# Performance work log

Measured on AMD Instinct MI355X. Metric: run time of the kernel, lower is better.

## Reference

```python
import jax, jax.numpy as jnp
import numpy as np

D_MODEL, H, D_FF = 1024, 16, 4096
B, S = 2, 2048
EPS = 1e-05


def layer_norm(x, gamma, beta):
    # Matches torch: mean and UNBIASED std over last dim, scalar gamma/beta,
    # and eps added to std (not variance).
    mean = jnp.mean(x, axis=-1, keepdims=True)
    var = jnp.sum((x - mean) ** 2, axis=-1, keepdims=True) / (x.shape[-1] - 1)
    return gamma * (x - mean) / (jnp.sqrt(var) + EPS) + beta


def setup_inputs() -> dict:
    key = jax.random.key(0)
    ks = jax.random.split(key, 16)
    sd = 1.0 / np.sqrt(D_MODEL)
    sf = 1.0 / np.sqrt(D_FF)
    return {
        "x": jax.random.normal(ks[0], (B, S, D_MODEL), jnp.float32),
        "mask": jnp.ones((1, 1, S, S), jnp.int32),
        "wq": jax.random.uniform(ks[1], (D_MODEL, D_MODEL), jnp.float32, -sd, sd),
        "bq": jax.random.uniform(ks[2], (D_MODEL,), jnp.float32, -sd, sd),
        "wk": jax.random.uniform(ks[3], (D_MODEL, D_MODEL), jnp.float32, -sd, sd),
        "bk": jax.random.uniform(ks[4], (D_MODEL,), jnp.float32, -sd, sd),
        "wv": jax.random.uniform(ks[5], (D_MODEL, D_MODEL), jnp.float32, -sd, sd),
        "bv": jax.random.uniform(ks[6], (D_MODEL,), jnp.float32, -sd, sd),
        "wo": jax.random.uniform(ks[7], (D_MODEL, D_MODEL), jnp.float32, -sd, sd),
        "bo": jax.random.uniform(ks[8], (D_MODEL,), jnp.float32, -sd, sd),
        "w1": jax.random.uniform(ks[9], (D_FF, D_MODEL), jnp.float32, -sd, sd),
        "b1": jax.random.uniform(ks[10], (D_FF,), jnp.float32, -sd, sd),
        "w2": jax.random.uniform(ks[11], (D_MODEL, D_FF), jnp.float32, -sf, sf),
        "b2": jax.random.uniform(ks[12], (D_MODEL,), jnp.float32, -sf, sf),
        "gamma1": jnp.ones((1,), jnp.float32),
        "beta1": jnp.zeros((1,), jnp.float32),
        "gamma2": jnp.ones((1,), jnp.float32),
        "beta2": jnp.zeros((1,), jnp.float32),
    }


def reference(x, mask, wq, bq, wk, bk, wv, bv, wo, bo, w1, b1, w2, b2,
              gamma1, beta1, gamma2, beta2):
    d_k = D_MODEL // H

    # --- residual 1: pre-LN self-attention ---
    xn = layer_norm(x, gamma1, beta1)
    q = (xn @ wq.T + bq).reshape(B, S, H, d_k).transpose(0, 2, 1, 3)
    k = (xn @ wk.T + bk).reshape(B, S, H, d_k).transpose(0, 2, 1, 3)
    v = (xn @ wv.T + bv).reshape(B, S, H, d_k).transpose(0, 2, 1, 3)

    scores = jnp.einsum("bhqd,bhkd->bhqk", q, k) / jnp.sqrt(
        jnp.asarray(d_k, x.dtype))
    scores = jnp.where(mask == 0, jnp.asarray(-1e9, x.dtype), scores)
    attn = jax.nn.softmax(scores, axis=-1)
    ctx = jnp.einsum("bhqk,bhkd->bhqd", attn, v)
    ctx = ctx.transpose(0, 2, 1, 3).reshape(B, S, D_MODEL)
    x = x + (ctx @ wo.T + bo)

    # --- residual 2: pre-LN feed-forward ---
    xn = layer_norm(x, gamma2, beta2)
    h = jax.nn.relu(xn @ w1.T + b1)
    x = x + (h @ w2.T + b2)
    return x
```

## Files before the change

### kernel.cpp

```cpp
#include <hip/hip_runtime.h>


typedef __bf16 bf16_t;
typedef __attribute__((ext_vector_type(8))) __bf16 bf16x8;
typedef __attribute__((ext_vector_type(4))) __bf16 bf16x4;
typedef __attribute__((ext_vector_type(2))) __bf16 bf16x2;
typedef __attribute__((ext_vector_type(4))) float f32x4;
typedef __attribute__((ext_vector_type(16))) float f32x16;
typedef __attribute__((ext_vector_type(2))) unsigned uint32x2;
typedef __attribute__((ext_vector_type(4))) unsigned uint32x4;

#define MB (1024ull * 1024ull)
#define QSCALE 0.18033688011112043f

__device__ __forceinline__ void gload_lds16(const bf16_t* g, bf16_t* l) {
    __builtin_amdgcn_global_load_lds(
        (const __attribute__((address_space(1))) void*)g,
        (__attribute__((address_space(3))) void*)l, 16, 0, 0);
}

__device__ __forceinline__ int bswz(int row) { return ((row >> 1) & 3) << 3; }

__device__ __forceinline__ int swz(int row, int col) {
    return row * 64 + ((((col >> 3) ^ row) & 7) << 3) + (col & 7);
}

__device__ __forceinline__ unsigned cvtpk(float a, float b) {
    bf16x2 v = {(__bf16)a, (__bf16)b};
    return __builtin_bit_cast(unsigned, v);
}

__global__ __launch_bounds__(256) void cvt_all(
    const float* __restrict__ wq, const float* __restrict__ wk,
    const float* __restrict__ wv, const float* __restrict__ wo,
    const float* __restrict__ w1, const float* __restrict__ w2,
    bf16_t* __restrict__ wqkv, bf16_t* __restrict__ wob, bf16_t* __restrict__ w1b,
    bf16_t* __restrict__ w2b) {
    const int b = blockIdx.x, t = threadIdx.x;
    const float* in;
    bf16_t* out;
    int i;
    if (b < 1024) { in = wq; out = wqkv; i = b * 256 + t; }
    else if (b < 2048) { in = wk; out = wqkv + 1048576; i = (b - 1024) * 256 + t; }
    else if (b < 3072) { in = wv; out = wqkv + 2097152; i = (b - 2048) * 256 + t; }
    else if (b < 4096) { in = wo; out = wob; i = (b - 3072) * 256 + t; }
    else if (b < 8192) { in = w1; out = w1b; i = (b - 4096) * 256 + t; }
    else { in = w2; out = w2b; i = (b - 8192) * 256 + t; }
    float4 v = ((const float4*)in)[i];
    bf16x4 o = {(__bf16)v.x, (__bf16)v.y, (__bf16)v.z, (__bf16)v.w};
    ((bf16x4*)out)[i] = o;
}

__global__ __launch_bounds__(256) void ln_kernel(const float* __restrict__ x,
                                                 bf16_t* __restrict__ out,
                                                 const float* __restrict__ gamma,
                                                 const float* __restrict__ beta) {
    const int lane = threadIdx.x & 63;
    const int row = blockIdx.x * 4 + (threadIdx.x >> 6);
    const float* xr = x + (size_t)row * 1024;
    float4 v[4];
    float s = 0.f;
#pragma unroll
    for (int i = 0; i < 4; ++i) {
        v[i] = ((const float4*)xr)[i * 64 + lane];
        s += v[i].x + v[i].y + v[i].z + v[i].w;
    }
#pragma unroll
    for (int o = 32; o; o >>= 1) s += __shfl_xor(s, o);
    float mean = s * (1.f / 1024.f);
    float vs = 0.f;
#pragma unroll
    for (int i = 0; i < 4; ++i) {
        float a = v[i].x - mean, b = v[i].y - mean, c = v[i].z - mean, d = v[i].w - mean;
        vs += a * a + b * b + c * c + d * d;
    }
#pragma unroll
    for (int o = 32; o; o >>= 1) vs += __shfl_xor(vs, o);
    float inv = 1.f / (sqrtf(vs * (1.f / 1023.f)) + 1e-5f);
    float g = gamma[0] * inv, bb = beta[0];
    bf16_t* orow = out + (size_t)row * 1024;
#pragma unroll
    for (int i = 0; i < 4; ++i) {
        bf16x4 ov = {(__bf16)((v[i].x - mean) * g + bb), (__bf16)((v[i].y - mean) * g + bb),
                     (__bf16)((v[i].z - mean) * g + bb), (__bf16)((v[i].w - mean) * g + bb)};
        *(bf16x4*)(orow + (i * 64 + lane) * 4) = ov;
    }
}

template <int KERN>
__global__ __launch_bounds__(512, 2) void gemm256(
    const bf16_t* __restrict__ A, const bf16_t* __restrict__ Bw, int K,
    const float* __restrict__ bias0, const float* __restrict__ bias1,
    const float* __restrict__ bias2, void* __restrict__ o0, void* __restrict__ o1,
    void* __restrict__ o2) {
    __shared__ bf16_t L[4 * 16384];
    const int t = threadIdx.x, lane = t & 63, w = t >> 6;
    const int wm = w >> 2, wn = w & 3;
    const int l15 = lane & 15, l4 = lane >> 4;
    const int bm = blockIdx.x, bn = blockIdx.y;
    const int NT = K >> 5;
    const bf16_t* Ab = A + (size_t)bm * 256 * K;
    const bf16_t* Bb = Bw + (size_t)bn * 256 * K;
    const int srow = t >> 2, pcol = (t & 3) * 8;
    f32x4 acc[8][4] = {};

    auto stageA = [&](int tt) {
        bf16_t* s = L + (tt & 3) * 16384;
        const int kb = tt * 32;
#pragma unroll
        for (int i = 0; i < 2; ++i) {
            int row = i * 128 + srow;
            int lcol = pcol ^ bswz(row);
            gload_lds16(Ab + (size_t)row * K + kb + lcol, s + i * 4096 + t * 8);
        }
    };
    auto stageB = [&](int tt) {
        bf16_t* s = L + (tt & 3) * 16384 + 8192;
        const int kb = tt * 32;
#pragma unroll
        for (int i = 0; i < 2; ++i) {
            int row = i * 128 + srow;
            int lcol = pcol ^ bswz(row);
            gload_lds16(Bb + (size_t)row * K + kb + lcol, s + i * 4096 + t * 8);
        }
    };

    stageA(0); stageB(0); stageA(1); stageB(1); stageA(2); stageB(2);
    asm volatile("s_waitcnt vmcnt(8)" ::: "memory");
    __builtin_amdgcn_s_barrier();

    for (int tt = 0; tt < NT; ++tt) {
        bf16_t* s = L + (tt & 3) * 16384;
        bf16_t* sB = s + 8192;
        bf16x8 af[4], bfr[4];
#pragma unroll
        for (int m = 0; m < 4; ++m) {
            int row = wm * 128 + m * 16 + l15;
            af[m] = *(const bf16x8*)(s + row * 32 + ((l4 * 8) ^ bswz(row)));
        }
#pragma unroll
        for (int n = 0; n < 4; ++n) {
            int row = wn * 64 + n * 16 + l15;
            bfr[n] = *(const bf16x8*)(sB + row * 32 + ((l4 * 8) ^ bswz(row)));
        }
        if (tt + 3 < NT) stageA(tt + 3);
        __builtin_amdgcn_s_barrier();
        __builtin_amdgcn_s_setprio(1);
#pragma unroll
        for (int m = 0; m < 4; ++m)
#pragma unroll
            for (int n = 0; n < 4; ++n)
                acc[m][n] = __builtin_amdgcn_mfma_f32_16x16x32_bf16(af[m], bfr[n], acc[m][n],
                                                                   0, 0, 0);
        __builtin_amdgcn_s_setprio(0);
        __builtin_amdgcn_s_barrier();
#pragma unroll
        for (int m = 0; m < 4; ++m) {
            int row = wm * 128 + 64 + m * 16 + l15;
            af[m] = *(const bf16x8*)(s + row * 32 + ((l4 * 8) ^ bswz(row)));
        }
        if (tt + 3 < NT) stageB(tt + 3);
        __builtin_amdgcn_s_barrier();
        __builtin_amdgcn_s_setprio(1);
#pragma unroll
        for (int m = 0; m < 4; ++m)
#pragma unroll
            for (int n = 0; n < 4; ++n)
                acc[4 + m][n] = __builtin_amdgcn_mfma_f32_16x16x32_bf16(af[m], bfr[n],
                                                                       acc[4 + m][n], 0, 0, 0);
        __builtin_amdgcn_s_setprio(0);
        if (tt + 3 < NT)
            asm volatile("s_waitcnt vmcnt(8)" ::: "memory");
        else if (tt + 2 < NT)
            asm volatile("s_waitcnt vmcnt(4)" ::: "memory");
        else
            asm volatile("s_waitcnt vmcnt(0)" ::: "memory");
        __builtin_amdgcn_s_barrier();
    }

    if (KERN == 1) {
        const int colb = bn * 256 + wn * 64;
        float bb[4];
#pragma unroll
        for (int n = 0; n < 4; ++n) bb[n] = bias0[colb + n * 16 + l15];
#pragma unroll
        for (int m = 0; m < 8; ++m) {
            const int row0 = bm * 256 + wm * 128 + m * 16 + (l4 << 2);
#pragma unroll
            for (int n = 0; n < 4; ++n)
#pragma unroll
                for (int j = 0; j < 4; ++j) {
                    float v = acc[m][n][j] + bb[n];
                    ((bf16_t*)o0)[(size_t)(row0 + j) * 4096 + colb + n * 16 + l15] =
                        (bf16_t)(v > 0.f ? v : 0.f);
                }
        }
        return;
    }
    if (bn < 8) {
        const bool isq = bn < 4;
        const float* bias = isq ? bias0 : bias1;
        const int head = (bn & 3) * 4 + wn;
        const int b = (bm * 256) >> 11;
        const int srow0 = (bm * 256 + wm * 128) & 2047;
        bf16_t* dst = (bf16_t*)(isq ? o0 : o1) + ((size_t)(b * 16 + head) << 17);
        float bb[4];
#pragma unroll
        for (int n = 0; n < 4; ++n) bb[n] = bias[head * 64 + n * 16 + l15];
#pragma unroll
        for (int m = 0; m < 8; ++m)
#pragma unroll
            for (int n = 0; n < 4; ++n)
#pragma unroll
                for (int j = 0; j < 4; ++j) {
                    int srw = srow0 + m * 16 + (l4 << 2) + j;
                    float v = acc[m][n][j] + bb[n];
                    if (isq) v *= QSCALE;
                    dst[((size_t)srw << 6) + n * 16 + l15] = (bf16_t)v;
                }
    } else {
        const int head = (bn - 8) * 4 + wn;
        const int b = (bm * 256) >> 11;
        const int sbase = (bm * 256 + wm * 128) & 2047;
        bf16_t* P = L + w * 8192;
        float bb[4];
#pragma unroll
        for (int n = 0; n < 4; ++n) bb[n] = bias2[head * 64 + n * 16 + l15];
#pragma unroll
        for (int m = 0; m < 8; ++m)
#pragma unroll
            for (int n = 0; n < 4; ++n) {
                int d = n * 16 + l15;
                int sl = m * 16 + (l4 << 2);
                bf16x4 pk = {(__bf16)(acc[m][n][0] + bb[n]), (__bf16)(acc[m][n][1] + bb[n]),
                             (__bf16)(acc[m][n][2] + bb[n]), (__bf16)(acc[m][n][3] + bb[n])};
                *(bf16x4*)(P + d * 128 + (sl ^ ((d & 7) << 3))) = pk;
            }
#pragma unroll
        for (int p = 0; p < 16; ++p) {
            int id = p * 64 + lane;
            int d = id >> 4, c8 = (id & 15) * 8;
            bf16x8 vv = *(const bf16x8*)(P + d * 128 + (c8 ^ ((d & 7) << 3)));
            *(bf16x8*)((bf16_t*)o2 + (((size_t)(b * 16 + head) * 64 + d) << 11) + sbase + c8) =
                vv;
        }
    }
}

template <int SPLIT>
__global__ __launch_bounds__(256, 2) void gemm128sq(
    const bf16_t* __restrict__ A, const bf16_t* __restrict__ Bw, int stride, int Ks,
    const float* __restrict__ bias, const float* __restrict__ resid,
    void* __restrict__ o0, void* __restrict__ o1) {
    __shared__ bf16_t L[4 * 8192];
    const int t = threadIdx.x, lane = t & 63, w = t >> 6;
    const int wr = w >> 1, wc = w & 1;
    const int l15 = lane & 15, l4 = lane >> 4;
    const int bm = blockIdx.x, bn = blockIdx.y;
    const int NT = Ks >> 5;
    const size_t kofs = SPLIT ? (size_t)blockIdx.z * Ks : 0;
    const bf16_t* Ab = A + (size_t)bm * 128 * stride + kofs;
    const bf16_t* Bb = Bw + (size_t)bn * 128 * stride + kofs;
    const int srow = t >> 2, pcol = (t & 3) * 8;
    f32x4 acc[4][4] = {};

    auto STAGE = [&](int tt) {
        bf16_t* s = L + (tt & 3) * 8192;
        const int kb = tt * 32;
#pragma unroll
        for (int i = 0; i < 2; ++i) {
            int row = i * 64 + srow;
            int lcol = pcol ^ bswz(row);
            gload_lds16(Ab + (size_t)row * stride + kb + lcol, s + i * 2048 + t * 8);
            gload_lds16(Bb + (size_t)row * stride + kb + lcol, s + 4096 + i * 2048 + t * 8);
        }
    };

    STAGE(0); STAGE(1); STAGE(2);
    asm volatile("s_waitcnt vmcnt(8)" ::: "memory");
    __builtin_amdgcn_s_barrier();

    for (int tt = 0; tt < NT; ++tt) {
        bf16_t* s = L + (tt & 3) * 8192;
        bf16x8 af[4], bfr[4];
#pragma unroll
        for (int m = 0; m < 4; ++m) {
            int row = wr * 64 + m * 16 + l15;
            af[m] = *(const bf16x8*)(s + row * 32 + ((l4 * 8) ^ bswz(row)));
        }
#pragma unroll
        for (int n = 0; n < 4; ++n) {
            int row = wc * 64 + n * 16 + l15;
            bfr[n] = *(const bf16x8*)(s + 4096 + row * 32 + ((l4 * 8) ^ bswz(row)));
        }
        if (tt + 3 < NT) STAGE(tt + 3);
        __builtin_amdgcn_s_barrier();
        __builtin_amdgcn_s_setprio(1);
#pragma unroll
        for (int m = 0; m < 4; ++m)
#pragma unroll
            for (int n = 0; n < 4; ++n)
                acc[m][n] = __builtin_amdgcn_mfma_f32_16x16x32_bf16(af[m], bfr[n], acc[m][n],
                                                                   0, 0, 0);
        __builtin_amdgcn_s_setprio(0);
        if (tt + 3 < NT)
            asm volatile("s_waitcnt vmcnt(8)" ::: "memory");
        else if (tt + 2 < NT)
            asm volatile("s_waitcnt vmcnt(4)" ::: "memory");
        else
            asm volatile("s_waitcnt vmcnt(0)" ::: "memory");
        __builtin_amdgcn_s_barrier();
    }

#pragma unroll
    for (int m = 0; m < 4; ++m) {
        const int row0 = bm * 128 + wr * 64 + m * 16 + (l4 << 2);
#pragma unroll
        for (int n = 0; n < 4; ++n) {
            const int col = bn * 128 + wc * 64 + n * 16 + l15;
#pragma unroll
            for (int j = 0; j < 4; ++j) {
                const int row = row0 + j;
                if (SPLIT == 0) {
                    ((float*)o0)[(size_t)row * 1024 + col] =
                        resid[(size_t)row * 1024 + col] + acc[m][n][j] + bias[col];
                } else {
                    bf16_t* po = (bf16_t*)(blockIdx.z ? o1 : o0);
                    po[(size_t)row * 1024 + col] = (bf16_t)acc[m][n][j];
                }
            }
        }
    }
}

__global__ __launch_bounds__(256) void ffn2_combine(
    const bf16_t* __restrict__ p0, const bf16_t* __restrict__ p1,
    const float* __restrict__ resid, const float* __restrict__ bias,
    float* __restrict__ out) {
    int i = blockIdx.x * 256 + threadIdx.x;
    float4 r = ((const float4*)resid)[i];
    bf16x4 a = ((const bf16x4*)p0)[i];
    bf16x4 b = ((const bf16x4*)p1)[i];
    float4 bs = ((const float4*)bias)[i & 255];
    float4 o;
    o.x = r.x + (float)a.x + (float)b.x + bs.x;
    o.y = r.y + (float)a.y + (float)b.y + bs.y;
    o.z = r.z + (float)a.z + (float)b.z + bs.z;
    o.w = r.w + (float)a.w + (float)b.w + bs.w;
    ((float4*)out)[i] = o;
}

__global__ __launch_bounds__(256, 4) void attn_split(const bf16_t* __restrict__ q,
                                                     const bf16_t* __restrict__ k,
                                                     const bf16_t* __restrict__ vt,
                                                     bf16_t* __restrict__ opart,
                                                     float2* __restrict__ ml) {
    __shared__ bf16_t Kl[2][64 * 64];
    __shared__ bf16_t Vl[2][64 * 64];
    const int t = threadIdx.x, lane = t & 63, w = t >> 6;
    const int bid = blockIdx.x;
    const int xcd = bid & 7, j = bid >> 3;
    const int bh = xcd + ((j >> 5) << 3);
    const int qx = (j & 31) >> 1;
    const int half = j & 1;
    const int sbase = half << 10;
    const bf16_t* qg = q + (size_t)bh * 2048 * 64;
    const bf16_t* kg = k + (size_t)bh * 2048 * 64;
    const bf16_t* vg = vt + (size_t)bh * 64 * 2048;
    const int l31 = lane & 31, h = lane >> 5;
    const int rowl = w * 32 + l31;
    const int qrow = qx * 128 + rowl;
    const int prow = t >> 3, p = t & 7;
    const int sc = ((p ^ prow) & 7) * 8;

    bf16x8 qf[4];
#pragma unroll
    for (int kd = 0; kd < 4; ++kd)
        qf[kd] = *(const bf16x8*)(qg + (size_t)qrow * 64 + kd * 16 + h * 8);

    f32x16 o0 = {}, o1 = {};
    float mi = -1e30f, li = 0.f;

    auto STAGE = [&](int tt) {
        bf16_t* kd_ = Kl[tt & 1];
        bf16_t* vd_ = Vl[tt & 1];
        const int kb = sbase + tt * 64;
        gload_lds16(kg + (size_t)(kb + prow) * 64 + sc, kd_ + t * 8);
        gload_lds16(kg + (size_t)(kb + prow + 32) * 64 + sc, kd_ + 2048 + t * 8);
        gload_lds16(vg + (size_t)prow * 2048 + kb + sc, vd_ + t * 8);
        gload_lds16(vg + (size_t)(prow + 32) * 2048 + kb + sc, vd_ + 2048 + t * 8);
    };

    STAGE(0);
    const int NT = 16;
    for (int tt = 0; tt < NT; ++tt) {
        if (tt + 1 < NT) {
            STAGE(tt + 1);
            asm volatile("s_waitcnt vmcnt(4)" ::: "memory");
        } else {
            asm volatile("s_waitcnt vmcnt(0)" ::: "memory");
        }
        __builtin_amdgcn_s_barrier();
        const bf16_t* Kb = Kl[tt & 1];
        const bf16_t* Vb = Vl[tt & 1];
        f32x16 sT0 = {}, sT1 = {};
        __builtin_amdgcn_s_setprio(1);
#pragma unroll
        for (int kd = 0; kd < 4; ++kd) {
            bf16x8 ka0 = *(const bf16x8*)(Kb + swz(l31, kd * 16 + h * 8));
            bf16x8 ka1 = *(const bf16x8*)(Kb + swz(32 + l31, kd * 16 + h * 8));
            sT0 = __builtin_amdgcn_mfma_f32_32x32x16_bf16(ka0, qf[kd], sT0, 0, 0, 0);
            sT1 = __builtin_amdgcn_mfma_f32_32x32x16_bf16(ka1, qf[kd], sT1, 0, 0, 0);
        }
        __builtin_amdgcn_s_setprio(0);
        float pm[16];
#pragma unroll
        for (int i = 0; i < 16; ++i) pm[i] = fmaxf(sT0[i], sT1[i]);
#pragma unroll
        for (int st = 8; st; st >>= 1)
#pragma unroll
            for (int i = 0; i < st; ++i) pm[i] = fmaxf(pm[i], pm[i + st]);
        float mx = fmaxf(pm[0], __shfl_xor(pm[0], 32));
        if (!__all(mx <= mi + 8.f)) {
            float mn = fmaxf(mi, mx);
            float al = __builtin_amdgcn_exp2f(mi - mn);
            mi = mn;
            li *= al;
            o0 *= al;
            o1 *= al;
        }
        f32x16 e0, e1;
#pragma unroll
        for (int i = 0; i < 16; ++i) e0[i] = __builtin_amdgcn_exp2f(sT0[i] - mi);
#pragma unroll
        for (int i = 0; i < 16; ++i) e1[i] = __builtin_amdgcn_exp2f(sT1[i] - mi);
        float ps[16];
#pragma unroll
        for (int i = 0; i < 16; ++i) ps[i] = e0[i] + e1[i];
#pragma unroll
        for (int st = 8; st; st >>= 1)
#pragma unroll
            for (int i = 0; i < st; ++i) ps[i] += ps[i + st];
        li += ps[0] + __shfl_xor(ps[0], 32);
        bf16x8 pa[4];
#pragma unroll
        for (int kd = 0; kd < 4; ++kd) {
            const f32x16& e = (kd < 2) ? e0 : e1;
            const int R0l = 8 * (kd & 1);
            const int R0h = R0l + 4;
            unsigned U0 = cvtpk(e[R0l + 0], e[R0l + 1]);
            unsigned V0 = cvtpk(e[R0l + 2], e[R0l + 3]);
            unsigned U1 = cvtpk(e[R0h + 0], e[R0h + 1]);
            unsigned V1 = cvtpk(e[R0h + 2], e[R0h + 3]);
            uint32x2 ru = __builtin_amdgcn_permlane32_swap(U0, U1, false, false);
            uint32x2 rv = __builtin_amdgcn_permlane32_swap(V0, V1, false, false);
            uint32x4 pw = {ru.x, rv.x, ru.y, rv.y};
            pa[kd] = __builtin_bit_cast(bf16x8, pw);
        }
        __builtin_amdgcn_s_setprio(1);
#pragma unroll
        for (int kd = 0; kd < 4; ++kd) {
            bf16x8 va0 = *(const bf16x8*)(Vb + swz(l31, kd * 16 + h * 8));
            bf16x8 va1 = *(const bf16x8*)(Vb + swz(32 + l31, kd * 16 + h * 8));
            o0 = __builtin_amdgcn_mfma_f32_32x32x16_bf16(va0, pa[kd], o0, 0, 0, 0);
            o1 = __builtin_amdgcn_mfma_f32_32x32x16_bf16(va1, pa[kd], o1, 0, 0, 0);
        }
        __builtin_amdgcn_s_setprio(0);
        __builtin_amdgcn_s_barrier();
    }
    const int combo = bh * 16 + qx;
    bf16_t* op = opart + ((size_t)half << 22) + (size_t)combo * 8192 + (size_t)rowl * 64;
#pragma unroll
    for (int g = 0; g < 4; ++g) {
        bf16x4 ov0 = {(__bf16)o0[4 * g + 0], (__bf16)o0[4 * g + 1], (__bf16)o0[4 * g + 2],
                      (__bf16)o0[4 * g + 3]};
        *(bf16x4*)(op + 8 * g + 4 * h) = ov0;
        bf16x4 ov1 = {(__bf16)o1[4 * g + 0], (__bf16)o1[4 * g + 1], (__bf16)o1[4 * g + 2],
                      (__bf16)o1[4 * g + 3]};
        *(bf16x4*)(op + 32 + 8 * g + 4 * h) = ov1;
    }
    if (h == 0) ml[((size_t)half * 512 + combo) * 128 + rowl] = make_float2(mi, li);
}

__global__ __launch_bounds__(256) void attn_merge(const bf16_t* __restrict__ opart,
                                                  const float2* __restrict__ ml,
                                                  bf16_t* __restrict__ ctx) {
    const int combo = blockIdx.x >> 2;
    const int row = (blockIdx.x & 3) * 32 + (threadIdx.x >> 3);
    const int d8 = (threadIdx.x & 7) * 8;
    float2 a = ml[(size_t)combo * 128 + row];
    float2 b = ml[(size_t)(512 + combo) * 128 + row];
    float m = fmaxf(a.x, b.x);
    float ea = __builtin_amdgcn_exp2f(a.x - m), eb = __builtin_amdgcn_exp2f(b.x - m);
    float inv = 1.f / (a.y * ea + b.y * eb);
    float ia = ea * inv, ib = eb * inv;
    size_t po = (size_t)combo * 8192 + (size_t)row * 64 + d8;
    bf16x8 u = *(const bf16x8*)(opart + po);
    bf16x8 v = *(const bf16x8*)(opart + (1ull << 22) + po);
    bf16x8 o;
#pragma unroll
    for (int jj = 0; jj < 8; ++jj) o[jj] = (__bf16)((float)u[jj] * ia + (float)v[jj] * ib);
    const int bh = combo >> 4, qx = combo & 15;
    const int rg = qx * 128 + row;
    *(bf16x8*)(ctx + ((size_t)(bh >> 4) * 2048 + rg) * 1024 + (bh & 15) * 64 + d8) = o;
}

extern "C" void kernel_launch(void* const* d_in, const int* in_sizes, int n_in,
                              void* d_out, int out_size, void* d_ws, size_t ws_size,
                              hipStream_t stream) {
    const float* x = (const float*)d_in[0];
    const float* wq = (const float*)d_in[2];
    const float* bq = (const float*)d_in[3];
    const float* wk = (const float*)d_in[4];
    const float* bk = (const float*)d_in[5];
    const float* wv = (const float*)d_in[6];
    const float* bv = (const float*)d_in[7];
    const float* wo = (const float*)d_in[8];
    const float* bo = (const float*)d_in[9];
    const float* w1 = (const float*)d_in[10];
    const float* b1 = (const float*)d_in[11];
    const float* w2 = (const float*)d_in[12];
    const float* b2 = (const float*)d_in[13];
    const float* gamma1 = (const float*)d_in[14];
    const float* beta1 = (const float*)d_in[15];
    const float* gamma2 = (const float*)d_in[16];
    const float* beta2 = (const float*)d_in[17];

    char* ws = (char*)d_ws;
    bf16_t* wqkv = (bf16_t*)(ws + 0);
    bf16_t* wob = (bf16_t*)(ws + 6 * MB);
    bf16_t* w1b = (bf16_t*)(ws + 8 * MB);
    bf16_t* w2b = (bf16_t*)(ws + 16 * MB);
    bf16_t* xnb = (bf16_t*)(ws + 24 * MB);
    bf16_t* qb = (bf16_t*)(ws + 32 * MB);
    bf16_t* kb = (bf16_t*)(ws + 40 * MB);
    bf16_t* vtb = (bf16_t*)(ws + 48 * MB);
    bf16_t* ctxb = (bf16_t*)(ws + 56 * MB);
    float* x1 = (float*)(ws + 64 * MB);
    bf16_t* hb = (bf16_t*)(ws + 32 * MB);
    bf16_t* opart = (bf16_t*)(ws + 64 * MB);
    float2* mlbuf = (float2*)(ws + 0);
    bf16_t* p0 = (bf16_t*)(ws + 0);
    bf16_t* p1 = (bf16_t*)(ws + 24 * MB);

    cvt_all<<<12288, 256, 0, stream>>>(wq, wk, wv, wo, w1, w2, wqkv, wob, w1b, w2b);

    ln_kernel<<<1024, 256, 0, stream>>>(x, xnb, gamma1, beta1);
    gemm256<0><<<dim3(16, 12), 512, 0, stream>>>(xnb, wqkv, 1024, bq, bk, bv, qb, kb, vtb);
    attn_split<<<1024, 256, 0, stream>>>(qb, kb, vtb, opart, mlbuf);
    attn_merge<<<2048, 256, 0, stream>>>(opart, mlbuf, ctxb);
    gemm128sq<0><<<dim3(32, 8), 256, 0, stream>>>(ctxb, wob, 1024, 1024, bo, x, x1, nullptr);
    ln_kernel<<<1024, 256, 0, stream>>>(x1, xnb, gamma2, beta2);
    gemm256<1><<<dim3(16, 16), 512, 0, stream>>>(xnb, w1b, 1024, b1, nullptr, nullptr, hb,
                                                 nullptr, nullptr);
    gemm128sq<1><<<dim3(32, 8, 2), 256, 0, stream>>>(hb, w2b, 4096, 2048, nullptr, nullptr,
                                                     p0, p1);
    ffn2_combine<<<4096, 256, 0, stream>>>(p0, p1, x1, b2, (float*)d_out);
}
```

Before: 219.4 us.

## Shrink big GEMM tile to 256x128 and switch GEMMs to double-buffered LDS

The QKV and FFN1 GEMMs now use 256x128 tiles with 8 waves of 64x64 each, which doubles the grid and cuts per-wave accumulators in half. Both GEMM kernels move from a 4-stage, 3-ahead LDS pipeline to a 2-stage double buffer with prefetch one tile ahead. The smaller LDS footprint and launch bounds raised to 4 blocks per CU are meant to increase occupancy. The trade-off is shallower prefetch, which exposes more global latency, and each B tile is now reused across fewer rows, which raises memory traffic.

```diff
diff --git a/kernel.cpp b/kernel.cpp
--- a/kernel.cpp
+++ b/kernel.cpp
@@ -19,7 +19,7 @@
         (__attribute__((address_space(3))) void*)l, 16, 0, 0);
 }
 
-__device__ __forceinline__ int bswz(int row) { return ((row >> 1) & 3) << 3; }
+__device__ __forceinline__ int bsw(int row) { return (row >> 1) & 3; }
 
 __device__ __forceinline__ int swz(int row, int col) {
     return row * 64 + ((((col >> 3) ^ row) & 7) << 3) + (col & 7);
@@ -88,63 +88,55 @@
 }
 
 template <int KERN>
-__global__ __launch_bounds__(512, 2) void gemm256(
+__global__ __launch_bounds__(512, 4) void gemmBig(
     const bf16_t* __restrict__ A, const bf16_t* __restrict__ Bw, int K,
     const float* __restrict__ bias0, const float* __restrict__ bias1,
     const float* __restrict__ bias2, void* __restrict__ o0, void* __restrict__ o1,
     void* __restrict__ o2) {
-    __shared__ bf16_t L[4 * 16384];
+    __shared__ bf16_t L[KERN == 0 ? 32768 : 24576];
     const int t = threadIdx.x, lane = t & 63, w = t >> 6;
-    const int wm = w >> 2, wn = w & 3;
+    const int wr = w >> 1, wc = w & 1;
     const int l15 = lane & 15, l4 = lane >> 4;
     const int bm = blockIdx.x, bn = blockIdx.y;
     const int NT = K >> 5;
     const bf16_t* Ab = A + (size_t)bm * 256 * K;
-    const bf16_t* Bb = Bw + (size_t)bn * 256 * K;
-    const int srow = t >> 2, pcol = (t & 3) * 8;
-    f32x4 acc[8][4] = {};
-
-    auto stageA = [&](int tt) {
-        bf16_t* s = L + (tt & 3) * 16384;
+    const bf16_t* Bb = Bw + (size_t)bn * 128 * K;
+    const int arow = t >> 1, ac0 = t & 1;
+    const int brow = t >> 2, bc = t & 3;
+    f32x4 acc[4][4] = {};
+
+    auto STAGE = [&](int tt) {
+        bf16_t* s = L + (tt & 1) * 12288;
         const int kb = tt * 32;
-#pragma unroll
-        for (int i = 0; i < 2; ++i) {
-            int row = i * 128 + srow;
-            int lcol = pcol ^ bswz(row);
-            gload_lds16(Ab + (size_t)row * K + kb + lcol, s + i * 4096 + t * 8);
-        }
+        gload_lds16(Ab + (size_t)arow * K + kb + ((ac0 ^ bsw(arow)) << 3), s + t * 8);
+        gload_lds16(Ab + (size_t)arow * K + kb + (((ac0 + 2) ^ bsw(arow)) << 3),
+                    s + 4096 + t * 8);
+        gload_lds16(Bb + (size_t)brow * K + kb + ((bc ^ bsw(brow)) << 3), s + 8192 + t * 8);
     };
-    auto stageB = [&](int tt) {
-        bf16_t* s = L + (tt & 3) * 16384 + 8192;
-        const int kb = tt * 32;
-#pragma unroll
-        for (int i = 0; i < 2; ++i) {
-            int row = i * 128 + srow;
-            int lcol = pcol ^ bswz(row);
-            gload_lds16(Bb + (size_t)row * K + kb + lcol, s + i * 4096 + t * 8);
-        }
-    };
-
-    stageA(0); stageB(0); stageA(1); stageB(1); stageA(2); stageB(2);
-    asm volatile("s_waitcnt vmcnt(8)" ::: "memory");
-    __builtin_amdgcn_s_barrier();
-
+
+    STAGE(0);
     for (int tt = 0; tt < NT; ++tt) {
-        bf16_t* s = L + (tt & 3) * 16384;
-        bf16_t* sB = s + 8192;
+        if (tt + 1 < NT) {
+            STAGE(tt + 1);
+            asm volatile("s_waitcnt vmcnt(3)" ::: "memory");
+        } else {
+            asm volatile("s_waitcnt vmcnt(0)" ::: "memory");
+        }
+        __builtin_amdgcn_s_barrier();
+        bf16_t* s = L + (tt & 1) * 12288;
         bf16x8 af[4], bfr[4];
 #pragma unroll
         for (int m = 0; m < 4; ++m) {
-            int row = wm * 128 + m * 16 + l15;
-            af[m] = *(const bf16x8*)(s + row * 32 + ((l4 * 8) ^ bswz(row)));
+            int row = wr * 64 + m * 16 + l15;
+            int ch = l4 ^ bsw(row);
+            af[m] = *(const bf16x8*)(s + ((ch >> 1) << 12) + row * 16 + ((ch & 1) << 3));
         }
 #pragma unroll
         for (int n = 0; n < 4; ++n) {
-            int row = wn * 64 + n * 16 + l15;
-            bfr[n] = *(const bf16x8*)(sB + row * 32 + ((l4 * 8) ^ bswz(row)));
-        }
-        if (tt + 3 < NT) stageA(tt + 3);
-        __builtin_amdgcn_s_barrier();
+            int row = wc * 64 + n * 16 + l15;
+            int ch = l4 ^ bsw(row);
+            bfr[n] = *(const bf16x8*)(s + 8192 + row * 32 + (ch << 3));
+        }
         __builtin_amdgcn_s_setprio(1);
 #pragma unroll
         for (int m = 0; m < 4; ++m)
@@ -154,38 +146,16 @@
                                                                    0, 0, 0);
         __builtin_amdgcn_s_setprio(0);
         __builtin_amdgcn_s_barrier();
+    }
+
+    if (KERN == 1) {
+        const int colb = bn * 128 + wc * 64;
+        float bb[4];
+#pragma unroll
+        for (int n = 0; n < 4; ++n) bb[n] = bias0[colb + n * 16 + l15];
 #pragma unroll
         for (int m = 0; m < 4; ++m) {
-            int row = wm * 128 + 64 + m * 16 + l15;
-            af[m] = *(const bf16x8*)(s + row * 32 + ((l4 * 8) ^ bswz(row)));
-        }
-        if (tt + 3 < NT) stageB(tt + 3);
-        __builtin_amdgcn_s_barrier();
-        __builtin_amdgcn_s_setprio(1);
-#pragma unroll
-        for (int m = 0; m < 4; ++m)
-#pragma unroll
-            for (int n = 0; n < 4; ++n)
-                acc[4 + m][n] = __builtin_amdgcn_mfma_f32_16x16x32_bf16(af[m], bfr[n],
-                                                                       acc[4 + m][n], 0, 0, 0);
-        __builtin_amdgcn_s_setprio(0);
-        if (tt + 3 < NT)
-            asm volatile("s_waitcnt vmcnt(8)" ::: "memory");
-        else if (tt + 2 < NT)
-            asm volatile("s_waitcnt vmcnt(4)" ::: "memory");
-        else
-            asm volatile("s_waitcnt vmcnt(0)" ::: "memory");
-        __builtin_amdgcn_s_barrier();
-    }
-
-    if (KERN == 1) {
-        const int colb = bn * 256 + wn * 64;
-        float bb[4];
-#pragma unroll
-        for (int n = 0; n < 4; ++n) bb[n] = bias0[colb + n * 16 + l15];
-#pragma unroll
-        for (int m = 0; m < 8; ++m) {
-            const int row0 = bm * 256 + wm * 128 + m * 16 + (l4 << 2);
+            const int row0 = bm * 256 + wr * 64 + m * 16 + (l4 << 2);
 #pragma unroll
             for (int n = 0; n < 4; ++n)
 #pragma unroll
@@ -197,62 +167,63 @@
         }
         return;
     }
-    if (bn < 8) {
-        const bool isq = bn < 4;
+    if (bn < 16) {
+        const bool isq = bn < 8;
         const float* bias = isq ? bias0 : bias1;
-        const int head = (bn & 3) * 4 + wn;
-        const int b = (bm * 256) >> 11;
-        const int srow0 = (bm * 256 + wm * 128) & 2047;
-        bf16_t* dst = (bf16_t*)(isq ? o0 : o1) + ((size_t)(b * 16 + head) << 17);
+        const int head = ((bn & 7) << 1) + wc;
+        bf16_t* dst = (bf16_t*)(isq ? o0 : o1);
         float bb[4];
 #pragma unroll
         for (int n = 0; n < 4; ++n) bb[n] = bias[head * 64 + n * 16 + l15];
 #pragma unroll
-        for (int m = 0; m < 8; ++m)
+        for (int m = 0; m < 4; ++m)
 #pragma unroll
             for (int n = 0; n < 4; ++n)
 #pragma unroll
                 for (int j = 0; j < 4; ++j) {
-                    int srw = srow0 + m * 16 + (l4 << 2) + j;
+                    int srw = bm * 256 + wr * 64 + m * 16 + (l4 << 2) + j;
+                    int b = srw >> 11, ss = srw & 2047;
                     float v = acc[m][n][j] + bb[n];
                     if (isq) v *= QSCALE;
-                    dst[((size_t)srw << 6) + n * 16 + l15] = (bf16_t)v;
+                    dst[((size_t)(b * 16 + head) << 17) + ((size_t)ss << 6) + n * 16 + l15] =
+                        (bf16_t)v;
                 }
     } else {
-        const int head = (bn - 8) * 4 + wn;
-        const int b = (bm * 256) >> 11;
-        const int sbase = (bm * 256 + wm * 128) & 2047;
-        bf16_t* P = L + w * 8192;
+        const int head = ((bn - 16) << 1) + wc;
+        const int srw0 = bm * 256 + wr * 64;
+        const int b = srw0 >> 11, sb = srw0 & 2047;
+        bf16_t* P = L + w * 4096;
         float bb[4];
 #pragma unroll
         for (int n = 0; n < 4; ++n) bb[n] = bias2[head * 64 + n * 16 + l15];
 #pragma unroll
-        for (int m = 0; m < 8; ++m)
+        for (int m = 0; m < 4; ++m)
 #pragma unroll
             for (int n = 0; n < 4; ++n) {
                 int d = n * 16 + l15;
-                int sl = m * 16 + (l4 << 2);
-                bf16x4 pk = {(__bf16)(acc[m][n][0] + bb[n]), (__bf16)(acc[m][n][1] + bb[n]),
-                             (__bf16)(acc[m][n][2] + bb[n]), (__bf16)(acc[m][n][3] + bb[n])};
-                *(bf16x4*)(P + d * 128 + (sl ^ ((d & 7) << 3))) = pk;
+#pragma unroll
+                for (int j = 0; j < 4; ++j) {
+                    int sl = m * 16 + (l4 << 2) + j;
+                    P[swz(d, sl)] = (bf16_t)(acc[m][n][j] + bb[n]);
+                }
             }
 #pragma unroll
-        for (int p = 0; p < 16; ++p) {
+        for (int p = 0; p < 8; ++p) {
             int id = p * 64 + lane;
-            int d = id >> 4, c8 = (id & 15) * 8;
-            bf16x8 vv = *(const bf16x8*)(P + d * 128 + (c8 ^ ((d & 7) << 3)));
-            *(bf16x8*)((bf16_t*)o2 + (((size_t)(b * 16 + head) * 64 + d) << 11) + sbase + c8) =
+            int d = id >> 3, c8 = (id & 7) * 8;
+            bf16x8 vv = *(const bf16x8*)(P + swz(d, c8));
+            *(bf16x8*)((bf16_t*)o2 + (((size_t)((b * 16 + head) * 64 + d)) << 11) + sb + c8) =
                 vv;
         }
     }
 }
 
 template <int SPLIT>
-__global__ __launch_bounds__(256, 2) void gemm128sq(
+__global__ __launch_bounds__(256, 4) void gemm128sq(
     const bf16_t* __restrict__ A, const bf16_t* __restrict__ Bw, int stride, int Ks,
     const float* __restrict__ bias, const float* __restrict__ resid,
     void* __restrict__ o0, void* __restrict__ o1) {
-    __shared__ bf16_t L[4 * 8192];
+    __shared__ bf16_t L[2 * 8192];
     const int t = threadIdx.x, lane = t & 63, w = t >> 6;
     const int wr = w >> 1, wc = w & 1;
     const int l15 = lane & 15, l4 = lane >> 4;
@@ -261,40 +232,42 @@
     const size_t kofs = SPLIT ? (size_t)blockIdx.z * Ks : 0;
     const bf16_t* Ab = A + (size_t)bm * 128 * stride + kofs;
     const bf16_t* Bb = Bw + (size_t)bn * 128 * stride + kofs;
-    const int srow = t >> 2, pcol = (t & 3) * 8;
+    const int srow = t >> 2, pcol = (t & 3);
     f32x4 acc[4][4] = {};
 
     auto STAGE = [&](int tt) {
-        bf16_t* s = L + (tt & 3) * 8192;
+        bf16_t* s = L + (tt & 1) * 8192;
         const int kb = tt * 32;
 #pragma unroll
         for (int i = 0; i < 2; ++i) {
             int row = i * 64 + srow;
-            int lcol = pcol ^ bswz(row);
+            int lcol = (pcol ^ bsw(row)) << 3;
             gload_lds16(Ab + (size_t)row * stride + kb + lcol, s + i * 2048 + t * 8);
             gload_lds16(Bb + (size_t)row * stride + kb + lcol, s + 4096 + i * 2048 + t * 8);
         }
     };
 
-    STAGE(0); STAGE(1); STAGE(2);
-    asm volatile("s_waitcnt vmcnt(8)" ::: "memory");
-    __builtin_amdgcn_s_barrier();
-
+    STAGE(0);
     for (int tt = 0; tt < NT; ++tt) {
-        bf16_t* s = L + (tt & 3) * 8192;
+        if (tt + 1 < NT) {
+            STAGE(tt + 1);
+            asm volatile("s_waitcnt vmcnt(4)" ::: "memory");
+        } else {
+            asm volatile("s_waitcnt vmcnt(0)" ::: "memory");
+        }
+        __builtin_amdgcn_s_barrier();
+        bf16_t* s = L + (tt & 1) * 8192;
         bf16x8 af[4], bfr[4];
 #pragma unroll
         for (int m = 0; m < 4; ++m) {
             int row = wr * 64 + m * 16 + l15;
-            af[m] = *(const bf16x8*)(s + row * 32 + ((l4 * 8) ^ bswz(row)));
+            af[m] = *(const bf16x8*)(s + row * 32 + (((l4 ^ bsw(row))) << 3));
         }
 #pragma unroll
         for (int n = 0; n < 4; ++n) {
             int row = wc * 64 + n * 16 + l15;
-            bfr[n] = *(const bf16x8*)(s + 4096 + row * 32 + ((l4 * 8) ^ bswz(row)));
-        }
-        if (tt + 3 < NT) STAGE(tt + 3);
-        __builtin_amdgcn_s_barrier();
+            bfr[n] = *(const bf16x8*)(s + 4096 + row * 32 + (((l4 ^ bsw(row))) << 3));
+        }
         __builtin_amdgcn_s_setprio(1);
 #pragma unroll
         for (int m = 0; m < 4; ++m)
@@ -303,12 +276,6 @@
                 acc[m][n] = __builtin_amdgcn_mfma_f32_16x16x32_bf16(af[m], bfr[n], acc[m][n],
                                                                    0, 0, 0);
         __builtin_amdgcn_s_setprio(0);
-        if (tt + 3 < NT)
-            asm volatile("s_waitcnt vmcnt(8)" ::: "memory");
-        else if (tt + 2 < NT)
-            asm volatile("s_waitcnt vmcnt(4)" ::: "memory");
-        else
-            asm volatile("s_waitcnt vmcnt(0)" ::: "memory");
         __builtin_amdgcn_s_barrier();
     }
 
@@ -546,12 +513,12 @@
     cvt_all<<<12288, 256, 0, stream>>>(wq, wk, wv, wo, w1, w2, wqkv, wob, w1b, w2b);
 
     ln_kernel<<<1024, 256, 0, stream>>>(x, xnb, gamma1, beta1);
-    gemm256<0><<<dim3(16, 12), 512, 0, stream>>>(xnb, wqkv, 1024, bq, bk, bv, qb, kb, vtb);
+    gemmBig<0><<<dim3(16, 24), 512, 0, stream>>>(xnb, wqkv, 1024, bq, bk, bv, qb, kb, vtb);
     attn_split<<<1024, 256, 0, stream>>>(qb, kb, vtb, opart, mlbuf);
     attn_merge<<<2048, 256, 0, stream>>>(opart, mlbuf, ctxb);
     gemm128sq<0><<<dim3(32, 8), 256, 0, stream>>>(ctxb, wob, 1024, 1024, bo, x, x1, nullptr);
     ln_kernel<<<1024, 256, 0, stream>>>(x1, xnb, gamma2, beta2);
-    gemm256<1><<<dim3(16, 16), 512, 0, stream>>>(xnb, w1b, 1024, b1, nullptr, nullptr, hb,
+    gemmBig<1><<<dim3(16, 32), 512, 0, stream>>>(xnb, w1b, 1024, b1, nullptr, nullptr, hb,
                                                  nullptr, nullptr);
     gemm128sq<1><<<dim3(32, 8, 2), 256, 0, stream>>>(hb, w2b, 4096, 2048, nullptr, nullptr,
                                                      p0, p1);
```

Result: slower. 224.2 us (+2.2%).

## Replace split-KV attention and merge pass with single full-sequence attention kernel

Applied to the files above, without the earlier changes.

Drops the two-way key-sequence split: each block now processes all 32 key tiles for its query tile and normalizes by the softmax denominator before writing ctx directly. This removes the separate merge kernel launch and the round trip of partial outputs and max/sum statistics through global memory. In exchange the grid halves from 1024 to 512 blocks, each doing twice as much sequential work, which lowers parallelism across CUs.

```diff
diff --git a/kernel.cpp b/kernel.cpp
--- a/kernel.cpp
+++ b/kernel.cpp
@@ -350,20 +350,17 @@
     ((float4*)out)[i] = o;
 }
 
-__global__ __launch_bounds__(256, 4) void attn_split(const bf16_t* __restrict__ q,
-                                                     const bf16_t* __restrict__ k,
-                                                     const bf16_t* __restrict__ vt,
-                                                     bf16_t* __restrict__ opart,
-                                                     float2* __restrict__ ml) {
+__global__ __launch_bounds__(256, 4) void attn_kernel(const bf16_t* __restrict__ q,
+                                                      const bf16_t* __restrict__ k,
+                                                      const bf16_t* __restrict__ vt,
+                                                      bf16_t* __restrict__ ctx) {
     __shared__ bf16_t Kl[2][64 * 64];
     __shared__ bf16_t Vl[2][64 * 64];
     const int t = threadIdx.x, lane = t & 63, w = t >> 6;
     const int bid = blockIdx.x;
     const int xcd = bid & 7, j = bid >> 3;
-    const int bh = xcd + ((j >> 5) << 3);
-    const int qx = (j & 31) >> 1;
-    const int half = j & 1;
-    const int sbase = half << 10;
+    const int bh = xcd + ((j >> 4) << 3);
+    const int qx = j & 15;
     const bf16_t* qg = q + (size_t)bh * 2048 * 64;
     const bf16_t* kg = k + (size_t)bh * 2048 * 64;
     const bf16_t* vg = vt + (size_t)bh * 64 * 2048;
@@ -384,7 +381,7 @@
     auto STAGE = [&](int tt) {
         bf16_t* kd_ = Kl[tt & 1];
         bf16_t* vd_ = Vl[tt & 1];
-        const int kb = sbase + tt * 64;
+        const int kb = tt * 64;
         gload_lds16(kg + (size_t)(kb + prow) * 64 + sc, kd_ + t * 8);
         gload_lds16(kg + (size_t)(kb + prow + 32) * 64 + sc, kd_ + 2048 + t * 8);
         gload_lds16(vg + (size_t)prow * 2048 + kb + sc, vd_ + t * 8);
@@ -392,7 +389,7 @@
     };
 
     STAGE(0);
-    const int NT = 16;
+    const int NT = 32;
     for (int tt = 0; tt < NT; ++tt) {
         if (tt + 1 < NT) {
             STAGE(tt + 1);
@@ -468,41 +465,17 @@
         __builtin_amdgcn_s_setprio(0);
         __builtin_amdgcn_s_barrier();
     }
-    const int combo = bh * 16 + qx;
-    bf16_t* op = opart + ((size_t)half << 22) + (size_t)combo * 8192 + (size_t)rowl * 64;
+    float inv = 1.f / li;
+    size_t base = ((size_t)(bh >> 4) * 2048 + qrow) * 1024 + (bh & 15) * 64;
 #pragma unroll
     for (int g = 0; g < 4; ++g) {
-        bf16x4 ov0 = {(__bf16)o0[4 * g + 0], (__bf16)o0[4 * g + 1], (__bf16)o0[4 * g + 2],
-                      (__bf16)o0[4 * g + 3]};
-        *(bf16x4*)(op + 8 * g + 4 * h) = ov0;
-        bf16x4 ov1 = {(__bf16)o1[4 * g + 0], (__bf16)o1[4 * g + 1], (__bf16)o1[4 * g + 2],
-                      (__bf16)o1[4 * g + 3]};
-        *(bf16x4*)(op + 32 + 8 * g + 4 * h) = ov1;
-    }
-    if (h == 0) ml[((size_t)half * 512 + combo) * 128 + rowl] = make_float2(mi, li);
-}
-
-__global__ __launch_bounds__(256) void attn_merge(const bf16_t* __restrict__ opart,
-                                                  const float2* __restrict__ ml,
-                                                  bf16_t* __restrict__ ctx) {
-    const int combo = blockIdx.x >> 2;
-    const int row = (blockIdx.x & 3) * 32 + (threadIdx.x >> 3);
-    const int d8 = (threadIdx.x & 7) * 8;
-    float2 a = ml[(size_t)combo * 128 + row];
-    float2 b = ml[(size_t)(512 + combo) * 128 + row];
-    float m = fmaxf(a.x, b.x);
-    float ea = __builtin_amdgcn_exp2f(a.x - m), eb = __builtin_amdgcn_exp2f(b.x - m);
-    float inv = 1.f / (a.y * ea + b.y * eb);
-    float ia = ea * inv, ib = eb * inv;
-    size_t po = (size_t)combo * 8192 + (size_t)row * 64 + d8;
-    bf16x8 u = *(const bf16x8*)(opart + po);
-    bf16x8 v = *(const bf16x8*)(opart + (1ull << 22) + po);
-    bf16x8 o;
-#pragma unroll
-    for (int jj = 0; jj < 8; ++jj) o[jj] = (__bf16)((float)u[jj] * ia + (float)v[jj] * ib);
-    const int bh = combo >> 4, qx = combo & 15;
-    const int rg = qx * 128 + row;
-    *(bf16x8*)(ctx + ((size_t)(bh >> 4) * 2048 + rg) * 1024 + (bh & 15) * 64 + d8) = o;
+        bf16x4 ov0 = {(__bf16)(o0[4 * g + 0] * inv), (__bf16)(o0[4 * g + 1] * inv),
+                      (__bf16)(o0[4 * g + 2] * inv), (__bf16)(o0[4 * g + 3] * inv)};
+        *(bf16x4*)(ctx + base + 8 * g + 4 * h) = ov0;
+        bf16x4 ov1 = {(__bf16)(o1[4 * g + 0] * inv), (__bf16)(o1[4 * g + 1] * inv),
+                      (__bf16)(o1[4 * g + 2] * inv), (__bf16)(o1[4 * g + 3] * inv)};
+        *(bf16x4*)(ctx + base + 32 + 8 * g + 4 * h) = ov1;
+    }
 }
 
 extern "C" void kernel_launch(void* const* d_in, const int* in_sizes, int n_in,
@@ -538,8 +511,6 @@
     bf16_t* ctxb = (bf16_t*)(ws + 56 * MB);
     float* x1 = (float*)(ws + 64 * MB);
     bf16_t* hb = (bf16_t*)(ws + 32 * MB);
-    bf16_t* opart = (bf16_t*)(ws + 64 * MB);
-    float2* mlbuf = (float2*)(ws + 0);
     bf16_t* p0 = (bf16_t*)(ws + 0);
     bf16_t* p1 = (bf16_t*)(ws + 24 * MB);
 
@@ -547,8 +518,7 @@
 
     ln_kernel<<<1024, 256, 0, stream>>>(x, xnb, gamma1, beta1);
     gemm256<0><<<dim3(16, 12), 512, 0, stream>>>(xnb, wqkv, 1024, bq, bk, bv, qb, kb, vtb);
-    attn_split<<<1024, 256, 0, stream>>>(qb, kb, vtb, opart, mlbuf);
-    attn_merge<<<2048, 256, 0, stream>>>(opart, mlbuf, ctxb);
+    attn_kernel<<<512, 256, 0, stream>>>(qb, kb, vtb, ctxb);
     gemm128sq<0><<<dim3(32, 8), 256, 0, stream>>>(ctxb, wob, 1024, 1024, bo, x, x1, nullptr);
     ln_kernel<<<1024, 256, 0, stream>>>(x1, xnb, gamma2, beta2);
     gemm256<1><<<dim3(16, 16), 512, 0, stream>>>(xnb, w1b, 1024, b1, nullptr, nullptr, hb,
```

New measurement: 217.7 us. About the same (-0.8%).
